# Kernel optimization log

Hardware: AMD Instinct MI355X
Metric: run time of the kernel (lower is better)

## Reference

```python
import jax, jax.numpy as jnp
import numpy as np

EPS = 1e-05
RMS_EPS = 1e-06


def activation_quant(x, num_bits=8):
    # per-token (last-dim) abs-max int8 fake quant, computed in fp32
    qn = -(2 ** (num_bits - 1))
    qp = 2 ** (num_bits - 1) - 1
    xf = x.astype(jnp.float32)
    s = qp / jnp.clip(jnp.max(jnp.abs(xf), axis=-1, keepdims=True), EPS, None)
    return (jnp.clip(jnp.round(xf * s), qn, qp) / s).astype(x.dtype)


def weight_quant(w):
    # full-tensor abs-mean ternary fake quant
    wf = w.astype(jnp.float32)
    s = 1.0 / jnp.clip(jnp.mean(jnp.abs(wf)), EPS, None)
    return (jnp.clip(jnp.round(wf * s), -1.0, 1.0) / s).astype(w.dtype)


def bit_linear(x, w):
    # STE wrappers (identity in forward value, straight-through in grad)
    qx = x + jax.lax.stop_gradient(activation_quant(x) - x)
    qw = w + jax.lax.stop_gradient(weight_quant(w) - w)
    return jnp.einsum('bsh,oh->bso', qx, qw)


def rms_norm(x, weight, eps=RMS_EPS):
    xf = x.astype(jnp.float32)
    var = jnp.mean(xf * xf, axis=-1, keepdims=True)
    return weight * (xf * jax.lax.rsqrt(var + eps)).astype(x.dtype)


def setup_inputs() -> dict:
    key = jax.random.key(0)
    k1, k2, k3, k4 = jax.random.split(key, 4)
    B, S, H, I = 2, 2048, 2048, 8192
    scale = 1.0 / np.sqrt(H)
    return {
        'x': jax.random.normal(k1, (B, S, H), dtype=jnp.float32),
        'w_gate': jax.random.normal(k2, (I, H), dtype=jnp.float32) * scale,
        'w_up': jax.random.normal(k3, (I, H), dtype=jnp.float32) * scale,
        'w_down': jax.random.normal(k4, (H, I), dtype=jnp.float32) * (1.0 / np.sqrt(I)),
        'ln_weight': jnp.ones((I,), dtype=jnp.float32),
    }


def reference(x, w_gate, w_up, w_down, ln_weight):
    h = jax.nn.silu(bit_linear(x, w_gate)) * bit_linear(x, w_up)
    h = rms_norm(h, ln_weight)
    return bit_linear(h, w_down)
```

## Files before the change

kernel.cpp:

```cpp
#include <hip/hip_runtime.h>
#include <stdint.h>

typedef int v4i __attribute__((ext_vector_type(4)));

#define TOKENS 4096
#define HDIM   2048
#define IDIM   8192
#define WN     16777216
#define NBLK   512
#define BANDP  5e-7f

#define MFMA_I8 __builtin_amdgcn_mfma_i32_16x16x64_i8

static __device__ __forceinline__ void gload_lds16(const void* g, void* l) {
  __builtin_amdgcn_global_load_lds(
      (const __attribute__((address_space(1))) void*)(unsigned long long)(uintptr_t)g,
      (__attribute__((address_space(3))) void*)(unsigned)(uintptr_t)l,
      16, 0, 0);
}

static __device__ __forceinline__ double wsum64d(double v) {
#pragma unroll
  for (int m = 32; m; m >>= 1) v += __shfl_xor(v, m, 64);
  return v;
}
static __device__ __forceinline__ double wmax64d(double v) {
#pragma unroll
  for (int m = 32; m; m >>= 1) v = fmax(v, __shfl_xor(v, m, 64));
  return v;
}
static __device__ __forceinline__ float wmax64f(float v) {
#pragma unroll
  for (int m = 32; m; m >>= 1) v = fmaxf(v, __shfl_xor(v, m, 64));
  return v;
}

static __device__ __forceinline__ int q8f(float v, float s, float lo, float hi) {
  float p = v * s;
  return (int)fminf(fmaxf(rintf(p), lo), hi);
}
static __device__ __forceinline__ uint32_t packq_f(float4 v, float s) {
  int a = q8f(v.x, s, -128.f, 127.f);
  int b = q8f(v.y, s, -128.f, 127.f);
  int c = q8f(v.z, s, -128.f, 127.f);
  int d = q8f(v.w, s, -128.f, 127.f);
  return (uint32_t)((a & 255) | ((b & 255) << 8) | ((c & 255) << 16) | ((d & 255) << 24));
}

__global__ __launch_bounds__(256) void wsum_leaf(const float* __restrict__ wg,
                                                 const float* __restrict__ wu,
                                                 const float* __restrict__ wd,
                                                 float* __restrict__ part) {
  const float* w = blockIdx.y == 0 ? wg : (blockIdx.y == 1 ? wu : wd);
  int tid = threadIdx.x;
  int wv = tid >> 6, lane = tid & 63;
  int lf = lane >> 1, m = lane & 1;
  __shared__ float A[256], B[256];
  const float4* w4 = (const float4*)w;
#pragma unroll
  for (int p = 0; p < 2; ++p) {
    int leaf = wv * 64 + p * 32 + lf;
    size_t b4 = ((size_t)blockIdx.x * 256 + leaf) * 32;
    float4 v = w4[b4 + m];
    float r0 = fabsf(v.x), r1 = fabsf(v.y), r2 = fabsf(v.z), r3 = fabsf(v.w);
    for (int k = 1; k < 16; ++k) {
      float4 u = w4[b4 + m + 2 * k];
      r0 += fabsf(u.x); r1 += fabsf(u.y); r2 += fabsf(u.z); r3 += fabsf(u.w);
    }
    float s = (r0 + r1) + (r2 + r3);
    float o = __shfl_xor(s, 1, 64);
    if (m == 0) A[leaf] = s + o;
  }
  __syncthreads();
  float* src = A; float* dst = B;
  for (int n = 128; n >= 1; n >>= 1) {
    if (tid < n) dst[tid] = src[2 * tid] + src[2 * tid + 1];
    __syncthreads();
    float* t = src; src = dst; dst = t;
  }
  if (tid == 0) part[blockIdx.y * NBLK + blockIdx.x] = src[0];
}

__global__ __launch_bounds__(256) void wsum_final(const float* __restrict__ part,
                                                  float* __restrict__ wsc) {
  int t = blockIdx.x, tid = threadIdx.x;
  __shared__ float A[512], B[256];
  A[tid] = part[t * NBLK + tid];
  A[tid + 256] = part[t * NBLK + tid + 256];
  __syncthreads();
  float* src = A; float* dst = B;
  for (int n = 256; n >= 1; n >>= 1) {
    if (tid < n) dst[tid] = src[2 * tid] + src[2 * tid + 1];
    __syncthreads();
    float* tmp = src; src = dst; dst = tmp;
  }
  if (tid == 0) {
    float mean32 = src[0] / (float)WN;
    float m32 = fmaxf(mean32, 1e-5f);
    float s32 = 1.0f / m32;
    wsc[t] = s32;
    wsc[3 + t] = 1.0f / s32;
  }
}

__global__ __launch_bounds__(256) void wquant_kernel(const float* __restrict__ wg,
                                                     const float* __restrict__ wu,
                                                     const float* __restrict__ wd,
                                                     const float* __restrict__ wsc,
                                                     int8_t* __restrict__ qg,
                                                     int8_t* __restrict__ qu,
                                                     int8_t* __restrict__ qd) {
  int t = blockIdx.y;
  const float* w = t == 0 ? wg : (t == 1 ? wu : wd);
  int8_t* q = t == 0 ? qg : (t == 1 ? qu : qd);
  float s32 = wsc[t];
  const float4* w4 = (const float4*)w;
  uint32_t* q4 = (uint32_t*)q;
  const int n4 = WN / 4;
  for (int i = blockIdx.x * 256 + threadIdx.x; i < n4; i += gridDim.x * 256) {
    float4 v = w4[i];
    float vv[4] = {v.x, v.y, v.z, v.w};
    int o[4];
#pragma unroll
    for (int j = 0; j < 4; ++j) {
      float pf = fabsf(vv[j]) * s32;
      int q2 = 2 * (int)fminf(rintf(pf), 1.0f);
      if (fabsf(pf - 0.5f) < BANDP) q2 = 1;
      o[j] = (vv[j] < 0.0f) ? -q2 : q2;
    }
    q4[i] = (uint32_t)((o[0] & 255) | ((o[1] & 255) << 8) |
                       ((o[2] & 255) << 16) | ((o[3] & 255) << 24));
  }
}

__global__ __launch_bounds__(256) void xquant_kernel(const float* __restrict__ x,
                                                     int8_t* __restrict__ qx,
                                                     double* __restrict__ axd) {
  int row = blockIdx.x, tid = threadIdx.x;
  const float4* xr = (const float4*)(x + (size_t)row * HDIM);
  float4 v0 = xr[tid], v1 = xr[tid + 256];
  float m = fmaxf(fmaxf(fmaxf(fabsf(v0.x), fabsf(v0.y)), fmaxf(fabsf(v0.z), fabsf(v0.w))),
                  fmaxf(fmaxf(fabsf(v1.x), fabsf(v1.y)), fmaxf(fabsf(v1.z), fabsf(v1.w))));
  m = wmax64f(m);
  __shared__ float red[4];
  int wid = tid >> 6, lane = tid & 63;
  if (lane == 0) red[wid] = m;
  __syncthreads();
  float mm = fmaxf(fmaxf(red[0], red[1]), fmaxf(red[2], red[3]));
  float c32 = fmaxf(mm, 1e-5f);
  float s32 = 127.0f / c32;
  if (tid == 0) axd[row] = 1.0 / (double)s32;
  uint32_t* q4 = (uint32_t*)(qx + (size_t)row * HDIM);
  q4[tid] = packq_f(v0, s32);
  q4[tid + 256] = packq_f(v1, s32);
}

__global__ __launch_bounds__(512, 2) void gemm1_kernel(const int8_t* __restrict__ qx,
                                                       const int8_t* __restrict__ qg,
                                                       const int8_t* __restrict__ qu,
                                                       const float* __restrict__ wsc,
                                                       const double* __restrict__ axd,
                                                       float* __restrict__ h) {
  __shared__ char lds[98304];
  int tid = threadIdx.x, wid = tid >> 6, lane = tid & 63;
  int l15 = lane & 15, lgp = lane >> 4;
  int wr = wid >> 2, wc = wid & 3;
  int flat = blockIdx.y * 64 + blockIdx.x;
  int xcd = flat & 7, local = flat >> 3;
  int mt = local >> 3, nl = local & 7;
  int m0 = mt * 256, n0 = (xcd * 8 + nl) * 128;
  const int8_t* bA = qx + (size_t)m0 * HDIM;
  const int8_t* bG = qg + (size_t)n0 * HDIM;
  const int8_t* bU = qu + (size_t)n0 * HDIM;

  v4i accg[8][2], accu[8][2];
  v4i vzero = {0, 0, 0, 0};
#pragma unroll
  for (int i = 0; i < 8; ++i)
#pragma unroll
    for (int j = 0; j < 2; ++j) { accg[i][j] = vzero; accu[i][j] = vzero; }

  int aoff[8], goff[2], uoff[2];
#pragma unroll
  for (int i = 0; i < 8; ++i)
    aoff[i] = lgp * 4096 + (wr * 128 + i * 16 + l15) * 16;
#pragma unroll
  for (int i = 0; i < 2; ++i) {
    goff[i] = 16384 + lgp * 2048 + (wc * 32 + i * 16 + l15) * 16;
    uoff[i] = goff[i] + 8192;
  }

  int rA8 = tid & 255, sA = tid >> 8;
  int sdA0 = sA * 4096 + rA8 * 16;
  int sdA1 = sdA0 + 8192;
  const size_t gA = (size_t)rA8 * HDIM;
  int rG = tid & 127, sG = tid >> 7;
  int sdG = 16384 + sG * 2048 + rG * 16;
  const size_t gG = (size_t)rG * HDIM;

  const int NT = HDIM / 64;
#pragma unroll
  for (int t0 = 0; t0 < 2; ++t0) {
    int cb = t0 * 32768;
    size_t kt = (size_t)t0 * 64;
    gload_lds16(bA + gA + kt + sA * 16,        lds + cb + sdA0);
    gload_lds16(bA + gA + kt + 32 + sA * 16,   lds + cb + sdA1);
    gload_lds16(bG + gG + kt + sG * 16,        lds + cb + sdG);
    gload_lds16(bU + gG + kt + sG * 16,        lds + cb + sdG + 8192);
  }
  asm volatile("s_waitcnt vmcnt(4)" ::: "memory");
  __builtin_amdgcn_s_barrier();
  __builtin_amdgcn_sched_barrier(0);

  int c0 = 0, c1 = 32768, c2 = 65536;
  for (int t = 0; t < NT; ++t) {
    const bool pf = (t + 2 < NT);
    size_t kt2 = (size_t)(t + 2) * 64;
    v4i a0 = *(const v4i*)(lds + c0 + aoff[0]);
    v4i a1 = *(const v4i*)(lds + c0 + aoff[1]);
    v4i a2 = *(const v4i*)(lds + c0 + aoff[2]);
    v4i a3 = *(const v4i*)(lds + c0 + aoff[3]);
    v4i bg0 = *(const v4i*)(lds + c0 + goff[0]);
    v4i bg1 = *(const v4i*)(lds + c0 + goff[1]);
    if (pf) {
      gload_lds16(bA + gA + kt2 + sA * 16,      lds + c2 + sdA0);
      gload_lds16(bA + gA + kt2 + 32 + sA * 16, lds + c2 + sdA1);
    }
    __builtin_amdgcn_s_barrier();
    asm volatile("s_waitcnt lgkmcnt(0)" ::: "memory");
    __builtin_amdgcn_sched_barrier(0);
    __builtin_amdgcn_s_setprio(1);
    accg[0][0] = MFMA_I8(a0, bg0, accg[0][0], 0, 0, 0);
    accg[0][1] = MFMA_I8(a0, bg1, accg[0][1], 0, 0, 0);
    accg[1][0] = MFMA_I8(a1, bg0, accg[1][0], 0, 0, 0);
    accg[1][1] = MFMA_I8(a1, bg1, accg[1][1], 0, 0, 0);
    accg[2][0] = MFMA_I8(a2, bg0, accg[2][0], 0, 0, 0);
    accg[2][1] = MFMA_I8(a2, bg1, accg[2][1], 0, 0, 0);
    accg[3][0] = MFMA_I8(a3, bg0, accg[3][0], 0, 0, 0);
    accg[3][1] = MFMA_I8(a3, bg1, accg[3][1], 0, 0, 0);
    __builtin_amdgcn_s_setprio(0);
    __builtin_amdgcn_s_barrier();
    v4i a4 = *(const v4i*)(lds + c0 + aoff[4]);
    v4i a5 = *(const v4i*)(lds + c0 + aoff[5]);
    v4i a6 = *(const v4i*)(lds + c0 + aoff[6]);
    v4i a7 = *(const v4i*)(lds + c0 + aoff[7]);
    if (pf) gload_lds16(bG + gG + kt2 + sG * 16, lds + c2 + sdG);
    __builtin_amdgcn_s_barrier();
    asm volatile("s_waitcnt lgkmcnt(0)" ::: "memory");
    __builtin_amdgcn_sched_barrier(0);
    __builtin_amdgcn_s_setprio(1);
    accg[4][0] = MFMA_I8(a4, bg0, accg[4][0], 0, 0, 0);
    accg[4][1] = MFMA_I8(a4, bg1, accg[4][1], 0, 0, 0);
    accg[5][0] = MFMA_I8(a5, bg0, accg[5][0], 0, 0, 0);
    accg[5][1] = MFMA_I8(a5, bg1, accg[5][1], 0, 0, 0);
    accg[6][0] = MFMA_I8(a6, bg0, accg[6][0], 0, 0, 0);
    accg[6][1] = MFMA_I8(a6, bg1, accg[6][1], 0, 0, 0);
    accg[7][0] = MFMA_I8(a7, bg0, accg[7][0], 0, 0, 0);
    accg[7][1] = MFMA_I8(a7, bg1, accg[7][1], 0, 0, 0);
    __builtin_amdgcn_s_setprio(0);
    __builtin_amdgcn_s_barrier();
    v4i bu0 = *(const v4i*)(lds + c0 + uoff[0]);
    v4i bu1 = *(const v4i*)(lds + c0 + uoff[1]);
    if (pf) gload_lds16(bU + gG + kt2 + sG * 16, lds + c2 + sdG + 8192);
    __builtin_amdgcn_s_barrier();
    asm volatile("s_waitcnt lgkmcnt(0)" ::: "memory");
    __builtin_amdgcn_sched_barrier(0);
    __builtin_amdgcn_s_setprio(1);
    accu[0][0] = MFMA_I8(a0, bu0, accu[0][0], 0, 0, 0);
    accu[0][1] = MFMA_I8(a0, bu1, accu[0][1], 0, 0, 0);
    accu[1][0] = MFMA_I8(a1, bu0, accu[1][0], 0, 0, 0);
    accu[1][1] = MFMA_I8(a1, bu1, accu[1][1], 0, 0, 0);
    accu[2][0] = MFMA_I8(a2, bu0, accu[2][0], 0, 0, 0);
    accu[2][1] = MFMA_I8(a2, bu1, accu[2][1], 0, 0, 0);
    accu[3][0] = MFMA_I8(a3, bu0, accu[3][0], 0, 0, 0);
    accu[3][1] = MFMA_I8(a3, bu1, accu[3][1], 0, 0, 0);
    __builtin_amdgcn_s_setprio(0);
    __builtin_amdgcn_s_barrier();
    if (pf)
      asm volatile("s_waitcnt vmcnt(4)" ::: "memory");
    else
      asm volatile("s_waitcnt vmcnt(0)" ::: "memory");
    __builtin_amdgcn_s_barrier();
    __builtin_amdgcn_sched_barrier(0);
    __builtin_amdgcn_s_setprio(1);
    accu[4][0] = MFMA_I8(a4, bu0, accu[4][0], 0, 0, 0);
    accu[4][1] = MFMA_I8(a4, bu1, accu[4][1], 0, 0, 0);
    accu[5][0] = MFMA_I8(a5, bu0, accu[5][0], 0, 0, 0);
    accu[5][1] = MFMA_I8(a5, bu1, accu[5][1], 0, 0, 0);
    accu[6][0] = MFMA_I8(a6, bu0, accu[6][0], 0, 0, 0);
    accu[6][1] = MFMA_I8(a6, bu1, accu[6][1], 0, 0, 0);
    accu[7][0] = MFMA_I8(a7, bu0, accu[7][0], 0, 0, 0);
    accu[7][1] = MFMA_I8(a7, bu1, accu[7][1], 0, 0, 0);
    __builtin_amdgcn_s_setprio(0);
    __builtin_amdgcn_s_barrier();
    int tmp = c0; c0 = c1; c1 = c2; c2 = tmp;
  }

  double mg = 0.5 * (double)wsc[3 + 0];
  double mu = 0.5 * (double)wsc[3 + 1];
#pragma unroll
  for (int mi = 0; mi < 8; ++mi) {
#pragma unroll
    for (int rg = 0; rg < 4; ++rg) {
      int grow = m0 + wr * 128 + mi * 16 + lgp * 4 + rg;
      double axr = axd[grow];
      double sg = axr * mg, su = axr * mu;
#pragma unroll
      for (int ni = 0; ni < 2; ++ni) {
        int gcol = n0 + wc * 32 + ni * 16 + l15;
        double g = (double)accg[mi][ni][rg] * sg;
        double u = (double)accu[mi][ni][rg] * su;
        double sig = 1.0 / (1.0 + exp(-g));
        h[(size_t)grow * IDIM + gcol] = (float)((g * sig) * u);
      }
    }
  }
}

__global__ __launch_bounds__(256) void hquant_kernel(const float* __restrict__ h,
                                                     const float* __restrict__ lnw,
                                                     double* __restrict__ ahd,
                                                     int8_t* __restrict__ qh) {
  int row = blockIdx.x, tid = threadIdx.x;
  const float4* hr = (const float4*)(h + (size_t)row * IDIM);
  const float4* lw4 = (const float4*)lnw;
  float4 hv[8], wv[8];
  double ssq = 0.0;
#pragma unroll
  for (int i = 0; i < 8; ++i) {
    hv[i] = hr[tid + i * 256];
    wv[i] = lw4[tid + i * 256];
    ssq += (double)hv[i].x * hv[i].x + (double)hv[i].y * hv[i].y +
           (double)hv[i].z * hv[i].z + (double)hv[i].w * hv[i].w;
  }
  ssq = wsum64d(ssq);
  __shared__ double redd[4];
  __shared__ double redm[4];
  int wid = tid >> 6, lane = tid & 63;
  if (lane == 0) redd[wid] = ssq;
  __syncthreads();
  double tot = redd[0] + redd[1] + redd[2] + redd[3];
  double rd = 1.0 / sqrt(tot * (1.0 / (double)IDIM) + 1e-6);
  double mx = 0.0;
#pragma unroll
  for (int i = 0; i < 8; ++i) {
    double y0 = (double)wv[i].x * ((double)hv[i].x * rd);
    double y1 = (double)wv[i].y * ((double)hv[i].y * rd);
    double y2 = (double)wv[i].z * ((double)hv[i].z * rd);
    double y3 = (double)wv[i].w * ((double)hv[i].w * rd);
    mx = fmax(mx, fmax(fmax(fabs(y0), fabs(y1)), fmax(fabs(y2), fabs(y3))));
  }
  mx = wmax64d(mx);
  if (lane == 0) redm[wid] = mx;
  __syncthreads();
  double mm = fmax(fmax(redm[0], redm[1]), fmax(redm[2], redm[3]));
  float c32 = fmaxf((float)mm, 1e-5f);
  float s32 = 127.0f / c32;
  double sd = (double)s32;
  if (tid == 0) ahd[row] = 1.0 / (double)s32;
  uint32_t* q4 = (uint32_t*)(qh + (size_t)row * IDIM);
#pragma unroll
  for (int i = 0; i < 8; ++i) {
    double y0 = (double)wv[i].x * ((double)hv[i].x * rd);
    double y1 = (double)wv[i].y * ((double)hv[i].y * rd);
    double y2 = (double)wv[i].z * ((double)hv[i].z * rd);
    double y3 = (double)wv[i].w * ((double)hv[i].w * rd);
    int a = (int)fmin(fmax(rint(y0 * sd), -128.0), 127.0);
    int b = (int)fmin(fmax(rint(y1 * sd), -128.0), 127.0);
    int c = (int)fmin(fmax(rint(y2 * sd), -128.0), 127.0);
    int d = (int)fmin(fmax(rint(y3 * sd), -128.0), 127.0);
    q4[tid + i * 256] = (uint32_t)((a & 255) | ((b & 255) << 8) | ((c & 255) << 16) | ((d & 255) << 24));
  }
}

__global__ __launch_bounds__(512, 4) void gemm2_kernel(const int8_t* __restrict__ qh,
                                                       const int8_t* __restrict__ qd,
                                                       const float* __restrict__ wsc,
                                                       const double* __restrict__ ahd,
                                                       float* __restrict__ out) {
  extern __shared__ char lds[];
  int tid = threadIdx.x, wid = tid >> 6, lane = tid & 63;
  int l15 = lane & 15, lgp = lane >> 4;
  int wr = wid >> 2, wc = wid & 3;
  int flat = blockIdx.y * 16 + blockIdx.x;
  int xcd = flat & 7, local = flat >> 3;
  int mt = xcd * 4 + (local >> 4), nt = local & 15;
  int m0 = mt * 128, n0 = nt * 128;
  const int8_t* bA = qh + (size_t)m0 * IDIM;
  const int8_t* bB = qd + (size_t)n0 * IDIM;

  v4i acc[4][2];
  v4i vzero = {0, 0, 0, 0};
#pragma unroll
  for (int i = 0; i < 4; ++i)
#pragma unroll
    for (int j = 0; j < 2; ++j) acc[i][j] = vzero;

  int aoff[4], boff[2];
#pragma unroll
  for (int i = 0; i < 4; ++i)
    aoff[i] = lgp * 2048 + (wr * 64 + i * 16 + l15) * 16;
#pragma unroll
  for (int i = 0; i < 2; ++i)
    boff[i] = 8192 + lgp * 2048 + (wc * 32 + i * 16 + l15) * 16;

  int srow = tid & 127, sslab = tid >> 7;
  const size_t rA = (size_t)srow * IDIM;
  int sdst = sslab * 2048 + srow * 16;

  const int NT = IDIM / 64;
  {
    size_t k0 = (size_t)sslab * 16;
    gload_lds16(bA + rA + k0, lds + sdst);
    gload_lds16(bB + rA + k0, lds + sdst + 8192);
    size_t k1 = 64 + (size_t)sslab * 16;
    gload_lds16(bA + rA + k1, lds + 16384 + sdst);
    gload_lds16(bB + rA + k1, lds + 16384 + sdst + 8192);
  }
  asm volatile("s_waitcnt vmcnt(2)" ::: "memory");
  __builtin_amdgcn_s_barrier();
  __builtin_amdgcn_sched_barrier(0);

  int c0 = 0, c1 = 16384, c2 = 32768;
  for (int t = 0; t < NT; ++t) {
    const bool pf = (t + 2 < NT);
    size_t koff = (size_t)(t + 2) * 64 + sslab * 16;
    v4i a0 = *(const v4i*)(lds + c0 + aoff[0]);
    v4i a1 = *(const v4i*)(lds + c0 + aoff[1]);
    v4i b0 = *(const v4i*)(lds + c0 + boff[0]);
    v4i b1 = *(const v4i*)(lds + c0 + boff[1]);
    if (pf) gload_lds16(bA + rA + koff, lds + c2 + sdst);
    __builtin_amdgcn_s_barrier();
    asm volatile("s_waitcnt lgkmcnt(0)" ::: "memory");
    __builtin_amdgcn_sched_barrier(0);
    __builtin_amdgcn_s_setprio(1);
    acc[0][0] = MFMA_I8(a0, b0, acc[0][0], 0, 0, 0);
    acc[0][1] = MFMA_I8(a0, b1, acc[0][1], 0, 0, 0);
    acc[1][0] = MFMA_I8(a1, b0, acc[1][0], 0, 0, 0);
    acc[1][1] = MFMA_I8(a1, b1, acc[1][1], 0, 0, 0);
    __builtin_amdgcn_s_setprio(0);
    __builtin_amdgcn_s_barrier();
    v4i a2 = *(const v4i*)(lds + c0 + aoff[2]);
    v4i a3 = *(const v4i*)(lds + c0 + aoff[3]);
    if (pf) gload_lds16(bB + rA + koff, lds + c2 + sdst + 8192);
    if (pf)
      asm volatile("s_waitcnt vmcnt(2)" ::: "memory");
    else
      asm volatile("s_waitcnt vmcnt(0)" ::: "memory");
    __builtin_amdgcn_s_barrier();
    asm volatile("s_waitcnt lgkmcnt(0)" ::: "memory");
    __builtin_amdgcn_sched_barrier(0);
    __builtin_amdgcn_s_setprio(1);
    acc[2][0] = MFMA_I8(a2, b0, acc[2][0], 0, 0, 0);
    acc[2][1] = MFMA_I8(a2, b1, acc[2][1], 0, 0, 0);
    acc[3][0] = MFMA_I8(a3, b0, acc[3][0], 0, 0, 0);
    acc[3][1] = MFMA_I8(a3, b1, acc[3][1], 0, 0, 0);
    __builtin_amdgcn_s_setprio(0);
    __builtin_amdgcn_s_barrier();
    int tmp = c0; c0 = c1; c1 = c2; c2 = tmp;
  }

  double md = 0.5 * (double)wsc[3 + 2];
#pragma unroll
  for (int mi = 0; mi < 4; ++mi) {
#pragma unroll
    for (int rg = 0; rg < 4; ++rg) {
      int grow = m0 + wr * 64 + mi * 16 + lgp * 4 + rg;
      double sc = ahd[grow] * md;
#pragma unroll
      for (int ni = 0; ni < 2; ++ni) {
        int gcol = n0 + wc * 32 + ni * 16 + l15;
        out[(size_t)grow * HDIM + gcol] = (float)((double)acc[mi][ni][rg] * sc);
      }
    }
  }
}

extern "C" void kernel_launch(void* const* d_in, const int* in_sizes, int n_in,
                              void* d_out, int out_size, void* d_ws, size_t ws_size,
                              hipStream_t stream) {
  const float* x   = (const float*)d_in[0];
  const float* wg  = (const float*)d_in[1];
  const float* wu  = (const float*)d_in[2];
  const float* wd  = (const float*)d_in[3];
  const float* lnw = (const float*)d_in[4];
  float* out = (float*)d_out;
  char* ws = (char*)d_ws;

  size_t off = 0;
  auto alloc = [&](size_t b) { size_t o = off; off += (b + 255) & ~(size_t)255; return o; };
  size_t o_wsc  = alloc(8 * 4);
  size_t o_part = alloc(3 * NBLK * 4);
  size_t o_axd  = alloc((size_t)TOKENS * 8);
  size_t o_ahd  = alloc((size_t)TOKENS * 8);
  size_t o_qx   = alloc((size_t)TOKENS * HDIM);
  size_t o_qg   = alloc((size_t)IDIM * HDIM);
  size_t o_qu   = alloc((size_t)IDIM * HDIM);
  size_t o_qd   = alloc((size_t)HDIM * IDIM);
  size_t o_h    = alloc((size_t)TOKENS * IDIM * 4);
  (void)ws_size; (void)in_sizes; (void)n_in; (void)out_size; (void)o_qu;

  float* wsc  = (float*)(ws + o_wsc);
  float* part = (float*)(ws + o_part);
  double* axd = (double*)(ws + o_axd);
  double* ahd = (double*)(ws + o_ahd);
  int8_t* qx  = (int8_t*)(ws + o_qx);
  int8_t* qg  = (int8_t*)(ws + o_qg);
  int8_t* qu  = (int8_t*)(ws + o_qu);
  int8_t* qd  = (int8_t*)(ws + o_qd);
  int8_t* qh  = (int8_t*)(ws + o_qg);
  float* h    = (float*)(ws + o_h);

  wsum_leaf<<<dim3(NBLK, 3), 256, 0, stream>>>(wg, wu, wd, part);
  wsum_final<<<3, 256, 0, stream>>>(part, wsc);
  wquant_kernel<<<dim3(1024, 3), 256, 0, stream>>>(wg, wu, wd, wsc, qg, qu, qd);
  xquant_kernel<<<TOKENS, 256, 0, stream>>>(x, qx, axd);
  gemm1_kernel<<<dim3(IDIM / 128, TOKENS / 256), 512, 0, stream>>>(qx, qg, qu, wsc, axd, h);
  hquant_kernel<<<TOKENS, 256, 0, stream>>>(h, lnw, ahd, qh);
  gemm2_kernel<<<dim3(HDIM / 128, TOKENS / 128), 512, 3 * 16384, stream>>>(qh, qd, wsc, ahd, out);
}
```

Baseline: 461.1 us.

## Enlarge gemm2 M-tile to 256 and drop redundant barriers in GEMM loops

The down-projection GEMM now uses a 256x128 tile per block: each wave computes 8x2 MFMA tiles instead of 4x2, and the XCD-aware block mapping is reworked so neighbouring blocks share B columns. LDS use is now a static 72 KB triple buffer. This raises arithmetic intensity per loaded byte and halves the block count. In both gemm1 and gemm2 the trailing barrier after each MFMA group is removed, cutting sync overhead, at the cost of relying on the remaining barriers for LDS hazard safety. Occupancy drops from 4 to 2 blocks per CU.

```diff
diff --git a/kernel.cpp b/kernel.cpp
--- a/kernel.cpp
+++ b/kernel.cpp
@@ -239,7 +239,6 @@
     accg[3][0] = MFMA_I8(a3, bg0, accg[3][0], 0, 0, 0);
     accg[3][1] = MFMA_I8(a3, bg1, accg[3][1], 0, 0, 0);
     __builtin_amdgcn_s_setprio(0);
-    __builtin_amdgcn_s_barrier();
     v4i a4 = *(const v4i*)(lds + c0 + aoff[4]);
     v4i a5 = *(const v4i*)(lds + c0 + aoff[5]);
     v4i a6 = *(const v4i*)(lds + c0 + aoff[6]);
@@ -258,7 +257,6 @@
     accg[7][0] = MFMA_I8(a7, bg0, accg[7][0], 0, 0, 0);
     accg[7][1] = MFMA_I8(a7, bg1, accg[7][1], 0, 0, 0);
     __builtin_amdgcn_s_setprio(0);
-    __builtin_amdgcn_s_barrier();
     v4i bu0 = *(const v4i*)(lds + c0 + uoff[0]);
     v4i bu1 = *(const v4i*)(lds + c0 + uoff[1]);
     if (pf) gload_lds16(bU + gG + kt2 + sG * 16, lds + c2 + sdG + 8192);
@@ -275,7 +273,6 @@
     accu[3][0] = MFMA_I8(a3, bu0, accu[3][0], 0, 0, 0);
     accu[3][1] = MFMA_I8(a3, bu1, accu[3][1], 0, 0, 0);
     __builtin_amdgcn_s_setprio(0);
-    __builtin_amdgcn_s_barrier();
     if (pf)
       asm volatile("s_waitcnt vmcnt(4)" ::: "memory");
     else
@@ -292,7 +289,6 @@
     accu[7][0] = MFMA_I8(a7, bu0, accu[7][0], 0, 0, 0);
     accu[7][1] = MFMA_I8(a7, bu1, accu[7][1], 0, 0, 0);
     __builtin_amdgcn_s_setprio(0);
-    __builtin_amdgcn_s_barrier();
     int tmp = c0; c0 = c1; c1 = c2; c2 = tmp;
   }
 
@@ -373,63 +369,72 @@
   }
 }
 
-__global__ __launch_bounds__(512, 4) void gemm2_kernel(const int8_t* __restrict__ qh,
+__global__ __launch_bounds__(512, 2) void gemm2_kernel(const int8_t* __restrict__ qh,
                                                        const int8_t* __restrict__ qd,
                                                        const float* __restrict__ wsc,
                                                        const double* __restrict__ ahd,
                                                        float* __restrict__ out) {
-  extern __shared__ char lds[];
+  __shared__ char lds[73728];
   int tid = threadIdx.x, wid = tid >> 6, lane = tid & 63;
   int l15 = lane & 15, lgp = lane >> 4;
   int wr = wid >> 2, wc = wid & 3;
   int flat = blockIdx.y * 16 + blockIdx.x;
   int xcd = flat & 7, local = flat >> 3;
-  int mt = xcd * 4 + (local >> 4), nt = local & 15;
-  int m0 = mt * 128, n0 = nt * 128;
+  int mt = local >> 1, nl = local & 1;
+  int m0 = mt * 256, n0 = (xcd * 2 + nl) * 128;
   const int8_t* bA = qh + (size_t)m0 * IDIM;
   const int8_t* bB = qd + (size_t)n0 * IDIM;
 
-  v4i acc[4][2];
+  v4i acc[8][2];
   v4i vzero = {0, 0, 0, 0};
 #pragma unroll
-  for (int i = 0; i < 4; ++i)
+  for (int i = 0; i < 8; ++i)
 #pragma unroll
     for (int j = 0; j < 2; ++j) acc[i][j] = vzero;
 
-  int aoff[4], boff[2];
-#pragma unroll
-  for (int i = 0; i < 4; ++i)
-    aoff[i] = lgp * 2048 + (wr * 64 + i * 16 + l15) * 16;
+  int aoff[8], boff[2];
+#pragma unroll
+  for (int i = 0; i < 8; ++i)
+    aoff[i] = lgp * 4096 + (wr * 128 + i * 16 + l15) * 16;
 #pragma unroll
   for (int i = 0; i < 2; ++i)
-    boff[i] = 8192 + lgp * 2048 + (wc * 32 + i * 16 + l15) * 16;
-
-  int srow = tid & 127, sslab = tid >> 7;
-  const size_t rA = (size_t)srow * IDIM;
-  int sdst = sslab * 2048 + srow * 16;
+    boff[i] = 16384 + lgp * 2048 + (wc * 32 + i * 16 + l15) * 16;
+
+  int rA8 = tid & 255, sA = tid >> 8;
+  int sdA0 = sA * 4096 + rA8 * 16;
+  int sdA1 = sdA0 + 8192;
+  const size_t gA = (size_t)rA8 * IDIM;
+  int rG = tid & 127, sG = tid >> 7;
+  int sdB = 16384 + sG * 2048 + rG * 16;
+  const size_t gB = (size_t)rG * IDIM;
 
   const int NT = IDIM / 64;
-  {
-    size_t k0 = (size_t)sslab * 16;
-    gload_lds16(bA + rA + k0, lds + sdst);
-    gload_lds16(bB + rA + k0, lds + sdst + 8192);
-    size_t k1 = 64 + (size_t)sslab * 16;
-    gload_lds16(bA + rA + k1, lds + 16384 + sdst);
-    gload_lds16(bB + rA + k1, lds + 16384 + sdst + 8192);
-  }
-  asm volatile("s_waitcnt vmcnt(2)" ::: "memory");
+#pragma unroll
+  for (int t0 = 0; t0 < 2; ++t0) {
+    int cb = t0 * 24576;
+    size_t kt = (size_t)t0 * 64;
+    gload_lds16(bA + gA + kt + sA * 16,      lds + cb + sdA0);
+    gload_lds16(bA + gA + kt + 32 + sA * 16, lds + cb + sdA1);
+    gload_lds16(bB + gB + kt + sG * 16,      lds + cb + sdB);
+  }
+  asm volatile("s_waitcnt vmcnt(3)" ::: "memory");
   __builtin_amdgcn_s_barrier();
   __builtin_amdgcn_sched_barrier(0);
 
-  int c0 = 0, c1 = 16384, c2 = 32768;
+  int c0 = 0, c1 = 24576, c2 = 49152;
   for (int t = 0; t < NT; ++t) {
     const bool pf = (t + 2 < NT);
-    size_t koff = (size_t)(t + 2) * 64 + sslab * 16;
+    size_t kt2 = (size_t)(t + 2) * 64;
     v4i a0 = *(const v4i*)(lds + c0 + aoff[0]);
     v4i a1 = *(const v4i*)(lds + c0 + aoff[1]);
+    v4i a2 = *(const v4i*)(lds + c0 + aoff[2]);
+    v4i a3 = *(const v4i*)(lds + c0 + aoff[3]);
     v4i b0 = *(const v4i*)(lds + c0 + boff[0]);
     v4i b1 = *(const v4i*)(lds + c0 + boff[1]);
-    if (pf) gload_lds16(bA + rA + koff, lds + c2 + sdst);
+    if (pf) {
+      gload_lds16(bA + gA + kt2 + sA * 16,      lds + c2 + sdA0);
+      gload_lds16(bA + gA + kt2 + 32 + sA * 16, lds + c2 + sdA1);
+    }
     __builtin_amdgcn_s_barrier();
     asm volatile("s_waitcnt lgkmcnt(0)" ::: "memory");
     __builtin_amdgcn_sched_barrier(0);
@@ -438,34 +443,42 @@
     acc[0][1] = MFMA_I8(a0, b1, acc[0][1], 0, 0, 0);
     acc[1][0] = MFMA_I8(a1, b0, acc[1][0], 0, 0, 0);
     acc[1][1] = MFMA_I8(a1, b1, acc[1][1], 0, 0, 0);
+    acc[2][0] = MFMA_I8(a2, b0, acc[2][0], 0, 0, 0);
+    acc[2][1] = MFMA_I8(a2, b1, acc[2][1], 0, 0, 0);
+    acc[3][0] = MFMA_I8(a3, b0, acc[3][0], 0, 0, 0);
+    acc[3][1] = MFMA_I8(a3, b1, acc[3][1], 0, 0, 0);
     __builtin_amdgcn_s_setprio(0);
-    __builtin_amdgcn_s_barrier();
-    v4i a2 = *(const v4i*)(lds + c0 + aoff[2]);
-    v4i a3 = *(const v4i*)(lds + c0 + aoff[3]);
-    if (pf) gload_lds16(bB + rA + koff, lds + c2 + sdst + 8192);
+    v4i a4 = *(const v4i*)(lds + c0 + aoff[4]);
+    v4i a5 = *(const v4i*)(lds + c0 + aoff[5]);
+    v4i a6 = *(const v4i*)(lds + c0 + aoff[6]);
+    v4i a7 = *(const v4i*)(lds + c0 + aoff[7]);
+    if (pf) gload_lds16(bB + gB + kt2 + sG * 16, lds + c2 + sdB);
     if (pf)
-      asm volatile("s_waitcnt vmcnt(2)" ::: "memory");
+      asm volatile("s_waitcnt vmcnt(3)" ::: "memory");
     else
       asm volatile("s_waitcnt vmcnt(0)" ::: "memory");
     __builtin_amdgcn_s_barrier();
     asm volatile("s_waitcnt lgkmcnt(0)" ::: "memory");
     __builtin_amdgcn_sched_barrier(0);
     __builtin_amdgcn_s_setprio(1);
-    acc[2][0] = MFMA_I8(a2, b0, acc[2][0], 0, 0, 0);
-    acc[2][1] = MFMA_I8(a2, b1, acc[2][1], 0, 0, 0);
-    acc[3][0] = MFMA_I8(a3, b0, acc[3][0], 0, 0, 0);
-    acc[3][1] = MFMA_I8(a3, b1, acc[3][1], 0, 0, 0);
+    acc[4][0] = MFMA_I8(a4, b0, acc[4][0], 0, 0, 0);
+    acc[4][1] = MFMA_I8(a4, b1, acc[4][1], 0, 0, 0);
+    acc[5][0] = MFMA_I8(a5, b0, acc[5][0], 0, 0, 0);
+    acc[5][1] = MFMA_I8(a5, b1, acc[5][1], 0, 0, 0);
+    acc[6][0] = MFMA_I8(a6, b0, acc[6][0], 0, 0, 0);
+    acc[6][1] = MFMA_I8(a6, b1, acc[6][1], 0, 0, 0);
+    acc[7][0] = MFMA_I8(a7, b0, acc[7][0], 0, 0, 0);
+    acc[7][1] = MFMA_I8(a7, b1, acc[7][1], 0, 0, 0);
     __builtin_amdgcn_s_setprio(0);
-    __builtin_amdgcn_s_barrier();
     int tmp = c0; c0 = c1; c1 = c2; c2 = tmp;
   }
 
   double md = 0.5 * (double)wsc[3 + 2];
 #pragma unroll
-  for (int mi = 0; mi < 4; ++mi) {
+  for (int mi = 0; mi < 8; ++mi) {
 #pragma unroll
     for (int rg = 0; rg < 4; ++rg) {
-      int grow = m0 + wr * 64 + mi * 16 + lgp * 4 + rg;
+      int grow = m0 + wr * 128 + mi * 16 + lgp * 4 + rg;
       double sc = ahd[grow] * md;
 #pragma unroll
       for (int ni = 0; ni < 2; ++ni) {
@@ -517,5 +530,5 @@
   xquant_kernel<<<TOKENS, 256, 0, stream>>>(x, qx, axd);
   gemm1_kernel<<<dim3(IDIM / 128, TOKENS / 256), 512, 0, stream>>>(qx, qg, qu, wsc, axd, h);
   hquant_kernel<<<TOKENS, 256, 0, stream>>>(h, lnw, ahd, qh);
-  gemm2_kernel<<<dim3(HDIM / 128, TOKENS / 128), 512, 3 * 16384, stream>>>(qh, qd, wsc, ahd, out);
-}
+  gemm2_kernel<<<dim3(HDIM / 128, TOKENS / 256), 512, 0, stream>>>(qh, qd, wsc, ahd, out);
+}
```

Measured after the change: 463.9 us, median of 3. No clear change (+0.6%).
